# Performance work log

Measured on AMD Instinct MI355X. Metric: run time of the kernel, lower is better.

The kernel has to match this reference:

```python
import jax, jax.numpy as jnp
import numpy as np

TABLES = 2048
MIN_LEN, MAX_LEN = 16384, 49152  # avg ~32768 rows per table -> ~67M total


def setup_inputs() -> dict:
    rng = np.random.default_rng(0)
    lengths = rng.integers(MIN_LEN, MAX_LEN, size=TABLES).astype(np.int64)
    input_offset = np.concatenate([[0], np.cumsum(lengths)]).astype(np.int32)  # [tables+1]
    permute = rng.permutation(TABLES).astype(np.int32)                          # [tables]
    out_lengths = lengths[permute]
    output_offset = np.concatenate([[0], np.cumsum(out_lengths)]).astype(np.int32)  # [tables+1]
    output_size = int(output_offset[-1])
    return {
        "permute": jnp.asarray(permute),
        "input_offset": jnp.asarray(input_offset),
        "output_offset": jnp.asarray(output_offset),
        "output_size": output_size,
    }


def reference(permute, input_offset, output_offset, output_size):
    # Vectorized equivalent of the nested Python loop:
    # for each output position j, find its table t via searchsorted over the
    # output offsets, then out[j] = input_offset[permute[t]] + (j - output_offset[t]).
    j = jnp.arange(output_size, dtype=jnp.int32)                      # [output_size]
    t = jnp.searchsorted(output_offset, j, side="right") - 1          # table id per element
    out = input_offset[permute[t]] + (j - output_offset[t])
    return out.astype(jnp.int32)
```

## Files before the change

kernel.cpp:

```cpp
#include <hip/hip_runtime.h>


constexpr int BLOCK = 256;
constexpr int TILE  = 4096;

__global__ __launch_bounds__(BLOCK) void ramp_tiles(
    const int* __restrict__ permute,
    const int* __restrict__ input_offset,
    const int* __restrict__ output_offset,
    int* __restrict__ out,
    int tables, int out_size)
{
    const int s = blockIdx.x * TILE;
    if (s >= out_size) return;
    const int e = min(s + TILE, out_size);

    int lo = 0, hi = tables;
    while (hi - lo > 1) {
        const int mid = (lo + hi) >> 1;
        if (output_offset[mid] <= s) lo = mid; else hi = mid;
    }
    const int t        = lo;
    const int boundary = output_offset[t + 1];
    const int base0    = input_offset[permute[t]] - output_offset[t];
    int base1 = 0;
    if (boundary < e) base1 = input_offset[permute[t + 1]] - boundary;

    const int tid = threadIdx.x;
    int4* __restrict__ out4 = reinterpret_cast<int4*>(out);
    const int e4 = e & ~3;

    #pragma unroll
    for (int k = 0; k < TILE / (BLOCK * 4); ++k) {
        const int j = s + (k * BLOCK + tid) * 4;
        if (j < e4) {
            int4 v;
            v.x = ((j    ) < boundary ? base0 : base1) + j;
            v.y = ((j + 1) < boundary ? base0 : base1) + j + 1;
            v.z = ((j + 2) < boundary ? base0 : base1) + j + 2;
            v.w = ((j + 3) < boundary ? base0 : base1) + j + 3;
            out4[j >> 2] = v;
        }
    }

    const int jt = e4 + tid;
    if (jt < e) out[jt] = ((jt < boundary) ? base0 : base1) + jt;
}

extern "C" void kernel_launch(void* const* d_in, const int* in_sizes, int n_in,
                              void* d_out, int out_size, void* d_ws, size_t ws_size,
                              hipStream_t stream) {
    const int* permute       = (const int*)d_in[0];
    const int* input_offset  = (const int*)d_in[1];
    const int* output_offset = (const int*)d_in[2];
    int* out = (int*)d_out;
    const int tables = in_sizes[0];

    const int grid = (out_size + TILE - 1) / TILE;
    hipLaunchKernelGGL(ramp_tiles, dim3(grid), dim3(BLOCK), 0, stream,
                       permute, input_offset, output_offset, out, tables, out_size);
}
```

Baseline: 46.07 us.

## Use persistent blocks walking contiguous tile ranges with incremental table tracking

Caps the grid at 2048 blocks, and each block processes a contiguous range of tiles instead of one tile per block. Only the first tile does a binary search over output offsets; later tiles advance the table index incrementally. This aims to cut block launch overhead and the repeated binary-search loads, at the cost of fewer blocks in flight and a serial per-block loop.

```diff
diff --git a/kernel.cpp b/kernel.cpp
--- a/kernel.cpp
+++ b/kernel.cpp
@@ -3,48 +3,63 @@
 
 constexpr int BLOCK = 256;
 constexpr int TILE  = 4096;
+constexpr int MAX_BLOCKS = 2048;
 
-__global__ __launch_bounds__(BLOCK) void ramp_tiles(
+__global__ __launch_bounds__(BLOCK) void ramp_persist(
     const int* __restrict__ permute,
     const int* __restrict__ input_offset,
     const int* __restrict__ output_offset,
     int* __restrict__ out,
     int tables, int out_size)
 {
-    const int s = blockIdx.x * TILE;
-    if (s >= out_size) return;
-    const int e = min(s + TILE, out_size);
+    const int ntiles = (out_size + TILE - 1) / TILE;
+    const int nb     = gridDim.x;
+    const int per    = (ntiles + nb - 1) / nb;
+    const int tile0  = blockIdx.x * per;
+    const int tile1  = min(tile0 + per, ntiles);
+    if (tile0 >= tile1) return;
 
+    int s = tile0 * TILE;
     int lo = 0, hi = tables;
     while (hi - lo > 1) {
         const int mid = (lo + hi) >> 1;
         if (output_offset[mid] <= s) lo = mid; else hi = mid;
     }
-    const int t        = lo;
-    const int boundary = output_offset[t + 1];
-    const int base0    = input_offset[permute[t]] - output_offset[t];
-    int base1 = 0;
-    if (boundary < e) base1 = input_offset[permute[t + 1]] - boundary;
+    int t        = lo;
+    int boundary = output_offset[t + 1];
+    int base0    = input_offset[permute[t]] - output_offset[t];
 
     const int tid = threadIdx.x;
     int4* __restrict__ out4 = reinterpret_cast<int4*>(out);
-    const int e4 = e & ~3;
 
-    #pragma unroll
-    for (int k = 0; k < TILE / (BLOCK * 4); ++k) {
-        const int j = s + (k * BLOCK + tid) * 4;
-        if (j < e4) {
-            int4 v;
-            v.x = ((j    ) < boundary ? base0 : base1) + j;
-            v.y = ((j + 1) < boundary ? base0 : base1) + j + 1;
-            v.z = ((j + 2) < boundary ? base0 : base1) + j + 2;
-            v.w = ((j + 3) < boundary ? base0 : base1) + j + 3;
-            out4[j >> 2] = v;
+    for (int tl = tile0; tl < tile1; ++tl) {
+        s = tl * TILE;
+        const int e = min(s + TILE, out_size);
+
+        while (boundary <= s) {
+            ++t;
+            base0    = input_offset[permute[t]] - boundary;
+            boundary = output_offset[t + 1];
         }
+        int base1 = base0;
+        if (boundary < e) base1 = input_offset[permute[t + 1]] - boundary;
+
+        const int e4 = e & ~3;
+        #pragma unroll
+        for (int k = 0; k < TILE / (BLOCK * 4); ++k) {
+            const int j = s + (k * BLOCK + tid) * 4;
+            if (j < e4) {
+                int4 v;
+                v.x = ((j    ) < boundary ? base0 : base1) + j;
+                v.y = ((j + 1) < boundary ? base0 : base1) + j + 1;
+                v.z = ((j + 2) < boundary ? base0 : base1) + j + 2;
+                v.w = ((j + 3) < boundary ? base0 : base1) + j + 3;
+                out4[j >> 2] = v;
+            }
+        }
+        const int jt = e4 + tid;
+        if (jt < e) out[jt] = ((jt < boundary) ? base0 : base1) + jt;
     }
-
-    const int jt = e4 + tid;
-    if (jt < e) out[jt] = ((jt < boundary) ? base0 : base1) + jt;
 }
 
 extern "C" void kernel_launch(void* const* d_in, const int* in_sizes, int n_in,
@@ -56,7 +71,8 @@
     int* out = (int*)d_out;
     const int tables = in_sizes[0];
 
-    const int grid = (out_size + TILE - 1) / TILE;
-    hipLaunchKernelGGL(ramp_tiles, dim3(grid), dim3(BLOCK), 0, stream,
+    const int ntiles = (out_size + TILE - 1) / TILE;
+    const int grid   = ntiles < MAX_BLOCKS ? ntiles : MAX_BLOCKS;
+    hipLaunchKernelGGL(ramp_persist, dim3(grid), dim3(BLOCK), 0, stream,
                        permute, input_offset, output_offset, out, tables, out_size);
 }
```

New measurement: 48.01 us. 4.2% more time.
